# Performance work log

Hardware: AMD Instinct MI355X
Metric: run time of the kernel (lower is better)

Reference implementation:

```python
import jax, jax.numpy as jnp
import numpy as np

NUM_HEADS = 12
HEAD_DIM = 64
NPT = 1  # num_prefix_tokens

def _rot(x):
    # pairs (x0,x1) -> (-x1, x0), matching timm's rot()
    x2 = x.reshape(*x.shape[:-1], -1, 2)
    r = jnp.stack([-x2[..., 1], x2[..., 0]], axis=-1)
    return r.reshape(x.shape)

def _apply_rope_cat(x, rope):
    # rope: [N_rot, 2*hd] = sin||cos concatenated
    sin, cos = jnp.split(rope, 2, axis=-1)
    return x * cos + _rot(x) * sin

def setup_inputs() -> dict:
    key = jax.random.key(0)
    ks = jax.random.split(key, 7)
    B, N, C = 8, 4097, 768
    hd = HEAD_DIM
    x = jax.random.normal(ks[0], (B, N, C), jnp.float32)
    rope = jax.random.normal(ks[1], (N - NPT, 2 * hd), jnp.float32)
    qkv_w = jax.random.normal(ks[2], (3 * C, C), jnp.float32) * (C ** -0.5)
    q_bias = jax.random.normal(ks[3], (C,), jnp.float32) * 0.02
    v_bias = jax.random.normal(ks[4], (C,), jnp.float32) * 0.02
    proj_w = jax.random.normal(ks[5], (C, C), jnp.float32) * (C ** -0.5)
    proj_b = jax.random.normal(ks[6], (C,), jnp.float32) * 0.02
    return dict(x=x, rope=rope, qkv_w=qkv_w, q_bias=q_bias, v_bias=v_bias,
                proj_w=proj_w, proj_b=proj_b)

def reference(x, rope, qkv_w, q_bias, v_bias, proj_w, proj_b):
    B, N, C = x.shape
    H, hd = NUM_HEADS, HEAD_DIM
    # fused QKV with k_bias fixed at zero (non-trainable buffer)
    bias = jnp.concatenate([q_bias, jnp.zeros_like(q_bias), v_bias])
    qkv = x @ qkv_w.T + bias                            # [B,N,3C]
    qkv = qkv.reshape(B, N, 3, H, hd).transpose(2, 0, 3, 1, 4)
    q, k, v = qkv[0], qkv[1], qkv[2]                    # [B,H,N,hd]
    # RoPE on all tokens except the prefix (CLS) token
    q = jnp.concatenate([q[:, :, :NPT], _apply_rope_cat(q[:, :, NPT:], rope)], axis=2)
    k = jnp.concatenate([k[:, :, :NPT], _apply_rope_cat(k[:, :, NPT:], rope)], axis=2)
    # linear attention: kv = K^T V, then Q @ kv, normalized by hd*N
    kv = jnp.einsum('bhnd,bhne->bhde', k, v)            # [B,H,hd,hd]
    out = jnp.einsum('bhnd,bhde->bhne', q, kv) / hd / N # [B,H,N,hd]
    out = out.transpose(0, 2, 1, 3).reshape(B, N, C)
    return out @ proj_w.T + proj_b
```

## Files before the change

### kernel.cpp

```cpp
#include <hip/hip_runtime.h>
#include <hip/hip_bf16.h>

typedef __attribute__((ext_vector_type(8))) short short8;
typedef __attribute__((ext_vector_type(4))) float f32x4;

#define B_    8
#define N_    4097
#define C_    768
#define M_TOT (B_*N_)
#define K3    (3*C_)
#define CHUNKS 16
#define NSTEP 24

__device__ __forceinline__ float bf2f(unsigned short u) {
  union { unsigned int i; float f; } x; x.i = ((unsigned int)u) << 16; return x.f;
}
__device__ __forceinline__ unsigned short f2bf(float f) {
  union { float f; unsigned int i; } x; x.f = f;
  unsigned int i = x.i + 0x7fffu + ((x.i >> 16) & 1u);
  return (unsigned short)(i >> 16);
}
__device__ __forceinline__ void gload16(const void* g, void* l) {
  __builtin_amdgcn_global_load_lds(
      (const __attribute__((address_space(1))) void*)g,
      (__attribute__((address_space(3))) void*)l, 16, 0, 0);
}

__global__ __launch_bounds__(256) void cvt_kernel(const float* __restrict__ inx,
                                                  unsigned short* __restrict__ outx,
                                                  const float* __restrict__ inw,
                                                  unsigned short* __restrict__ outw,
                                                  long n4x, long n4tot) {
  long i = (long)blockIdx.x * blockDim.x + threadIdx.x;
  long stride = (long)gridDim.x * blockDim.x;
  for (; i < n4tot; i += stride) {
    const float4* src; ushort4* dst; long j;
    if (i < n4x) { src = (const float4*)inx; dst = (ushort4*)outx; j = i; }
    else         { src = (const float4*)inw; dst = (ushort4*)outw; j = i - n4x; }
    float4 v = src[j];
    ushort4 o;
    o.x = f2bf(v.x); o.y = f2bf(v.y); o.z = f2bf(v.z); o.w = f2bf(v.w);
    dst[j] = o;
  }
}

__global__ __launch_bounds__(512, 4) void gemm_qkv_rope(
    const unsigned short* __restrict__ A,
    const unsigned short* __restrict__ Bw,
    const float* __restrict__ rope,
    const float* __restrict__ qb,
    const float* __restrict__ vb,
    unsigned short* __restrict__ qkv)
{
  __shared__ __align__(16) char L[3*24576];
  const int tid  = threadIdx.x;
  const int wave = tid >> 6, lane = tid & 63;
  const int lr = lane & 15, lk = lane >> 4;
  const int wm = wave >> 2, wn = wave & 3;

  const int o = blockIdx.x;
  const int xcd = o & 7, loc = o >> 3;
  const int tile = (xcd < 1 ? xcd*290 : 290 + (xcd-1)*289) + loc;
  const int m0 = (tile % 257) * 128;
  const int n0 = (tile / 257) * 256;

  const int arow = tid >> 2, achk = tid & 3;
  const int am = min(m0 + arow, M_TOT-1);
  const unsigned short* gA  = A  + (long)am*768 + achk*8;
  const unsigned short* gB1 = Bw + (long)(n0 + arow)*768 + achk*8;
  const unsigned short* gB2 = Bw + (long)(n0 + arow + 128)*768 + achk*8;
  const int dA  = wave*1024;
  const int dB1 = 8192  + wave*1024;
  const int dB2 = 16384 + wave*1024;

  const int abase = (wm*64 + lr)*64 + lk*16;
  const int bbase = 8192 + (wn*64 + lr)*64 + lk*16;

  f32x4 acc[4][4];
#pragma unroll
  for (int i = 0; i < 4; ++i)
#pragma unroll
    for (int j = 0; j < 4; ++j) acc[i][j] = (f32x4){0.f,0.f,0.f,0.f};

  auto STAGE = [&](int buf, int kk) {
    char* sb = L + buf*24576;
    gload16(gA  + kk, sb + dA);
    gload16(gB1 + kk, sb + dB1);
    gload16(gB2 + kk, sb + dB2);
  };
  auto COMPUTE = [&](int buf) {
    const char* sb = L + buf*24576;
    short8 af[4], bfr[4];
#pragma unroll
    for (int mi = 0; mi < 4; ++mi)
      af[mi] = *(const short8*)(sb + abase + mi*1024);
#pragma unroll
    for (int ni = 0; ni < 4; ++ni)
      bfr[ni] = *(const short8*)(sb + bbase + ni*1024);
#pragma unroll
    for (int mi = 0; mi < 4; ++mi)
#pragma unroll
      for (int ni = 0; ni < 4; ++ni)
        acc[mi][ni] = __builtin_amdgcn_mfma_f32_16x16x32_bf16(af[mi], bfr[ni], acc[mi][ni], 0, 0, 0);
  };

  STAGE(0, 0);
  STAGE(1, 32);
  asm volatile("s_waitcnt vmcnt(3)" ::: "memory");
  __builtin_amdgcn_s_barrier();
  __builtin_amdgcn_sched_barrier(0);

  int cur = 0;
  for (int tt = 0; tt < NSTEP-2; ++tt) {
    int stg = cur + 2; if (stg >= 3) stg -= 3;
    STAGE(stg, (tt+2)*32);
    COMPUTE(cur);
    asm volatile("s_waitcnt vmcnt(3)" ::: "memory");
    __builtin_amdgcn_sched_barrier(0);
    __builtin_amdgcn_s_barrier();
    __builtin_amdgcn_sched_barrier(0);
    cur = (cur + 1 == 3) ? 0 : cur + 1;
  }
  COMPUTE(cur);
  asm volatile("s_waitcnt vmcnt(0)" ::: "memory");
  __builtin_amdgcn_sched_barrier(0);
  __builtin_amdgcn_s_barrier();
  __builtin_amdgcn_sched_barrier(0);
  cur = (cur + 1 == 3) ? 0 : cur + 1;
  COMPUTE(cur);

  const int which = n0 / 768;
  unsigned short* plane = qkv + (long)which*M_TOT*768;

  float biasv[4]; int withv[4]; int dv[4];
#pragma unroll
  for (int ni = 0; ni < 4; ++ni) {
    const int gc = n0 + wn*64 + ni*16 + lr;
    const int within = gc - which*768;
    withv[ni] = within;
    dv[ni] = within & 63;
    biasv[ni] = (which == 0) ? qb[within] : (which == 2 ? vb[within] : 0.f);
  }

  if (which == 2) {
#pragma unroll
    for (int mi = 0; mi < 4; ++mi)
#pragma unroll
      for (int r = 0; r < 4; ++r) {
        const int gm = m0 + wm*64 + mi*16 + lk*4 + r;
        if (gm < M_TOT) {
#pragma unroll
          for (int ni = 0; ni < 4; ++ni)
            plane[(long)gm*768 + withv[ni]] = f2bf(acc[mi][ni][r] + biasv[ni]);
        }
      }
  } else {
#pragma unroll
    for (int mi = 0; mi < 4; ++mi) {
#pragma unroll
      for (int r = 0; r < 4; ++r) {
        const int gm = m0 + wm*64 + mi*16 + lk*4 + r;
        const int ntok = gm % 4097;
        const bool valid = gm < M_TOT;
        const bool dorope = (ntok > 0) && valid;
        const float* rp = rope + (long)(ntok - 1)*128;
#pragma unroll
        for (int ni = 0; ni < 4; ++ni) {
          float v = acc[mi][ni][r] + biasv[ni];
          float pair = __shfl_xor(v, 1);
          float vo = v;
          if (dorope) {
            const float s = rp[dv[ni]], c = rp[64 + dv[ni]];
            const float rot = (dv[ni] & 1) ? pair : -pair;
            vo = v*c + rot*s;
          }
          if (valid) plane[(long)gm*768 + withv[ni]] = f2bf(vo);
        }
      }
    }
  }
}

__global__ __launch_bounds__(256) void kv_partial_kernel(
    const unsigned short* __restrict__ qkv, float* __restrict__ part)
{
  const int bh = blockIdx.y;
  const int b = bh / 12, h = bh % 12;
  const int chunk = blockIdx.x;
  const int per = (N_ + CHUNKS - 1) / CHUNKS;
  const int nst = chunk * per;
  const int nen = min(nst + per, N_);
  const unsigned short* Kpl = qkv + (long)M_TOT*768 + ((long)b*N_)*768 + h*64;
  const unsigned short* Vpl = qkv + (long)2*M_TOT*768 + ((long)b*N_)*768 + h*64;
  __shared__ unsigned short Kl[32*64];
  __shared__ unsigned short Vl[32*64];
  const int t = threadIdx.x;
  const int ty = t >> 4, tx = t & 15;
  const int lrow = t >> 3, lpc = t & 7;
  float acc[4][4] = {};
  for (int nb = nst; nb < nen; nb += 32) {
    const int cnt = min(32, nen - nb);
    __syncthreads();
    if (lrow < cnt) {
      *(uint4*)(Kl + lrow*64 + lpc*8) = *(const uint4*)(Kpl + (long)(nb + lrow)*768 + lpc*8);
      *(uint4*)(Vl + lrow*64 + lpc*8) = *(const uint4*)(Vpl + (long)(nb + lrow)*768 + lpc*8);
    }
    __syncthreads();
#pragma unroll 2
    for (int i = 0; i < cnt; ++i) {
      const ushort4 ku = *(const ushort4*)(Kl + i*64 + ty*4);
      const ushort4 vu = *(const ushort4*)(Vl + i*64 + tx*4);
      float kf[4] = {bf2f(ku.x), bf2f(ku.y), bf2f(ku.z), bf2f(ku.w)};
      float vf[4] = {bf2f(vu.x), bf2f(vu.y), bf2f(vu.z), bf2f(vu.w)};
#pragma unroll
      for (int a = 0; a < 4; ++a)
#pragma unroll
        for (int e = 0; e < 4; ++e) acc[a][e] += kf[a]*vf[e];
    }
  }
  float* dst = part + ((long)chunk*96 + bh)*4096 + (ty*4)*64 + tx*4;
#pragma unroll
  for (int a = 0; a < 4; ++a)
#pragma unroll
    for (int e = 0; e < 4; ++e) dst[a*64 + e] = acc[a][e];
}

__global__ __launch_bounds__(256) void mcomb_kernel(const float* __restrict__ part,
                                                    const float* __restrict__ pw,
                                                    unsigned short* __restrict__ McT) {
  const int blk = blockIdx.x;
  const int cs = blk & 1;
  const int h  = (blk >> 1) % 12;
  const int b  = blk / 24;
  const int bh = b*12 + h;
  __shared__ float kvs[64][65];
  const int t = threadIdx.x;
  const int d_own = t >> 2;
  const int eg = (t & 3) * 16;

  float4 a0 = {0,0,0,0}, a1 = {0,0,0,0}, a2 = {0,0,0,0}, a3 = {0,0,0,0};
  const float4* p4 = (const float4*)part;
#pragma unroll
  for (int ch = 0; ch < CHUNKS; ++ch) {
    const long base = ((long)ch*96 + bh)*1024 + d_own*16 + (t & 3)*4;
    float4 v0 = p4[base+0], v1 = p4[base+1], v2 = p4[base+2], v3 = p4[base+3];
    a0.x += v0.x; a0.y += v0.y; a0.z += v0.z; a0.w += v0.w;
    a1.x += v1.x; a1.y += v1.y; a1.z += v1.z; a1.w += v1.w;
    a2.x += v2.x; a2.y += v2.y; a2.z += v2.z; a2.w += v2.w;
    a3.x += v3.x; a3.y += v3.y; a3.z += v3.z; a3.w += v3.w;
  }
  kvs[eg+ 0][d_own] = a0.x; kvs[eg+ 1][d_own] = a0.y; kvs[eg+ 2][d_own] = a0.z; kvs[eg+ 3][d_own] = a0.w;
  kvs[eg+ 4][d_own] = a1.x; kvs[eg+ 5][d_own] = a1.y; kvs[eg+ 6][d_own] = a1.z; kvs[eg+ 7][d_own] = a1.w;
  kvs[eg+ 8][d_own] = a2.x; kvs[eg+ 9][d_own] = a2.y; kvs[eg+10][d_own] = a2.z; kvs[eg+11][d_own] = a2.w;
  kvs[eg+12][d_own] = a3.x; kvs[eg+13][d_own] = a3.y; kvs[eg+14][d_own] = a3.z; kvs[eg+15][d_own] = a3.w;
  __syncthreads();

  const int lane = t & 63;
  const int w    = t >> 6;
  float kvcol[64];
#pragma unroll
  for (int e = 0; e < 64; ++e) kvcol[e] = kvs[e][lane];

  const float scale = (float)(1.0/(64.0*4097.0));
  const int cbase = cs*384 + w*96;
  for (int i = 0; i < 96; ++i) {
    const int c = cbase + i;
    const float* pwrow = pw + (long)c*768 + h*64;
    float s = 0.f;
#pragma unroll
    for (int e = 0; e < 64; ++e) s += pwrow[e] * kvcol[e];
    McT[((long)b*768 + c)*768 + h*64 + lane] = f2bf(s * scale);
  }
}

__global__ __launch_bounds__(512, 4) void gemm_final(
    const unsigned short* __restrict__ qkv,
    const unsigned short* __restrict__ McT,
    const float* __restrict__ pb,
    float* __restrict__ out)
{
  __shared__ __align__(16) char L[3*24576];
  const int tid  = threadIdx.x;
  const int wave = tid >> 6, lane = tid & 63;
  const int lr = lane & 15, lk = lane >> 4;
  const int wm = wave >> 2, wn = wave & 3;

  const int o = blockIdx.x;
  const int xcd = o & 7, loc = o >> 3;
  const int b  = xcd;
  const int ct = loc / 33, mt = loc % 33;
  const int m0 = mt * 128;
  const int c0 = ct * 256;

  const int arow = tid >> 2, achk = tid & 3;
  const int am = min(m0 + arow, N_-1);
  const unsigned short* gA  = qkv + ((long)b*N_ + am)*768 + achk*8;
  const unsigned short* Bb  = McT + (long)b*768*768;
  const unsigned short* gB1 = Bb + (long)(c0 + arow)*768 + achk*8;
  const unsigned short* gB2 = Bb + (long)(c0 + arow + 128)*768 + achk*8;
  const int dA  = wave*1024;
  const int dB1 = 8192  + wave*1024;
  const int dB2 = 16384 + wave*1024;

  const int abase = (wm*64 + lr)*64 + lk*16;
  const int bbase = 8192 + (wn*64 + lr)*64 + lk*16;

  f32x4 acc[4][4];
#pragma unroll
  for (int i = 0; i < 4; ++i)
#pragma unroll
    for (int j = 0; j < 4; ++j) acc[i][j] = (f32x4){0.f,0.f,0.f,0.f};

  auto STAGE = [&](int buf, int kk) {
    char* sb = L + buf*24576;
    gload16(gA  + kk, sb + dA);
    gload16(gB1 + kk, sb + dB1);
    gload16(gB2 + kk, sb + dB2);
  };
  auto COMPUTE = [&](int buf) {
    const char* sb = L + buf*24576;
    short8 af[4], bfr[4];
#pragma unroll
    for (int mi = 0; mi < 4; ++mi)
      af[mi] = *(const short8*)(sb + abase + mi*1024);
#pragma unroll
    for (int ni = 0; ni < 4; ++ni)
      bfr[ni] = *(const short8*)(sb + bbase + ni*1024);
#pragma unroll
    for (int mi = 0; mi < 4; ++mi)
#pragma unroll
      for (int ni = 0; ni < 4; ++ni)
        acc[mi][ni] = __builtin_amdgcn_mfma_f32_16x16x32_bf16(af[mi], bfr[ni], acc[mi][ni], 0, 0, 0);
  };

  STAGE(0, 0);
  STAGE(1, 32);
  asm volatile("s_waitcnt vmcnt(3)" ::: "memory");
  __builtin_amdgcn_s_barrier();
  __builtin_amdgcn_sched_barrier(0);

  int cur = 0;
  for (int tt = 0; tt < NSTEP-2; ++tt) {
    int stg = cur + 2; if (stg >= 3) stg -= 3;
    STAGE(stg, (tt+2)*32);
    COMPUTE(cur);
    asm volatile("s_waitcnt vmcnt(3)" ::: "memory");
    __builtin_amdgcn_sched_barrier(0);
    __builtin_amdgcn_s_barrier();
    __builtin_amdgcn_sched_barrier(0);
    cur = (cur + 1 == 3) ? 0 : cur + 1;
  }
  COMPUTE(cur);
  asm volatile("s_waitcnt vmcnt(0)" ::: "memory");
  __builtin_amdgcn_sched_barrier(0);
  __builtin_amdgcn_s_barrier();
  __builtin_amdgcn_sched_barrier(0);
  cur = (cur + 1 == 3) ? 0 : cur + 1;
  COMPUTE(cur);

#pragma unroll
  for (int mi = 0; mi < 4; ++mi) {
#pragma unroll
    for (int ni = 0; ni < 4; ++ni) {
      const int gc = c0 + wn*64 + ni*16 + lr;
      const float bias = pb[gc];
#pragma unroll
      for (int r = 0; r < 4; ++r) {
        const int tok = m0 + wm*64 + mi*16 + lk*4 + r;
        if (tok < N_)
          out[((long)b*N_ + tok)*768 + gc] = acc[mi][ni][r] + bias;
      }
    }
  }
}

extern "C" void kernel_launch(void* const* d_in, const int* in_sizes, int n_in,
                              void* d_out, int out_size, void* d_ws, size_t ws_size,
                              hipStream_t stream) {
  const float* x      = (const float*)d_in[0];
  const float* rope   = (const float*)d_in[1];
  const float* qkv_w  = (const float*)d_in[2];
  const float* q_bias = (const float*)d_in[3];
  const float* v_bias = (const float*)d_in[4];
  const float* proj_w = (const float*)d_in[5];
  const float* proj_b = (const float*)d_in[6];
  float* out = (float*)d_out;

  char* w0 = (char*)d_ws;
  unsigned short* x_bf  = (unsigned short*)w0;
  unsigned short* wq_bf = (unsigned short*)(w0 + 50343936);
  unsigned short* qkv   = (unsigned short*)(w0 + 50343936 + 3538944);
  float*          part  = (float*)w0;
  unsigned short* McT   = (unsigned short*)(w0 + 25165824 + 1572864);

  const long n4x = (long)M_TOT*768/4;
  const long n4w = (long)K3*768/4;
  cvt_kernel<<<2048, 256, 0, stream>>>(x, x_bf, qkv_w, wq_bf, n4x, n4x + n4w);

  gemm_qkv_rope<<<2313, 512, 0, stream>>>(x_bf, wq_bf, rope, q_bias, v_bias, qkv);

  kv_partial_kernel<<<dim3(CHUNKS, 96), 256, 0, stream>>>(qkv, part);
  mcomb_kernel<<<192, 256, 0, stream>>>(part, proj_w, McT);

  gemm_final<<<792, 512, 0, stream>>>(qkv, McT, proj_b, out);
}
```

Measured before the change: 438.1 us.

## Reorder LDS tile layout to MFMA fragment order, swap tile raster, use nontemporal stores

Both GEMM kernels now stage A/B tiles into LDS so that each wave's 16-row by 32-k block is stored contiguously in lane order. Fragment reads become linear per lane, which is meant to avoid LDS bank conflicts. The tile index mapping changes from M-major to N-major within each XCD, so neighbouring blocks reuse the same A rows in L2. Output stores use nontemporal hints to reduce cache pollution, which risks slower re-reads of qkv by later kernels.

```diff
diff --git a/kernel.cpp b/kernel.cpp
--- a/kernel.cpp
+++ b/kernel.cpp
@@ -61,20 +61,21 @@
   const int o = blockIdx.x;
   const int xcd = o & 7, loc = o >> 3;
   const int tile = (xcd < 1 ? xcd*290 : 290 + (xcd-1)*289) + loc;
-  const int m0 = (tile % 257) * 128;
-  const int n0 = (tile / 257) * 256;
-
-  const int arow = tid >> 2, achk = tid & 3;
+  const int m0 = (tile / 9) * 128;
+  const int n0 = (tile % 9) * 256;
+
+  const int arow = wave*16 + lr;
+  const int achk = lk;
   const int am = min(m0 + arow, M_TOT-1);
   const unsigned short* gA  = A  + (long)am*768 + achk*8;
   const unsigned short* gB1 = Bw + (long)(n0 + arow)*768 + achk*8;
-  const unsigned short* gB2 = Bw + (long)(n0 + arow + 128)*768 + achk*8;
-  const int dA  = wave*1024;
-  const int dB1 = 8192  + wave*1024;
-  const int dB2 = 16384 + wave*1024;
-
-  const int abase = (wm*64 + lr)*64 + lk*16;
-  const int bbase = 8192 + (wn*64 + lr)*64 + lk*16;
+  const unsigned short* gB2 = Bw + (long)(n0 + 128 + arow)*768 + achk*8;
+  const int dA  = tid*16;
+  const int dB1 = 8192  + tid*16;
+  const int dB2 = 16384 + tid*16;
+
+  const int abase = (wm*4)*1024 + lane*16;
+  const int bbase = 8192 + (wn*4)*1024 + lane*16;
 
   f32x4 acc[4][4];
 #pragma unroll
@@ -151,7 +152,8 @@
         if (gm < M_TOT) {
 #pragma unroll
           for (int ni = 0; ni < 4; ++ni)
-            plane[(long)gm*768 + withv[ni]] = f2bf(acc[mi][ni][r] + biasv[ni]);
+            __builtin_nontemporal_store(f2bf(acc[mi][ni][r] + biasv[ni]),
+                                        plane + (long)gm*768 + withv[ni]);
         }
       }
   } else {
@@ -174,7 +176,8 @@
             const float rot = (dv[ni] & 1) ? pair : -pair;
             vo = v*c + rot*s;
           }
-          if (valid) plane[(long)gm*768 + withv[ni]] = f2bf(vo);
+          if (valid)
+            __builtin_nontemporal_store(f2bf(vo), plane + (long)gm*768 + withv[ni]);
         }
       }
     }
@@ -288,22 +291,23 @@
   const int o = blockIdx.x;
   const int xcd = o & 7, loc = o >> 3;
   const int b  = xcd;
-  const int ct = loc / 33, mt = loc % 33;
+  const int mt = loc / 3, ct = loc % 3;
   const int m0 = mt * 128;
   const int c0 = ct * 256;
 
-  const int arow = tid >> 2, achk = tid & 3;
+  const int arow = wave*16 + lr;
+  const int achk = lk;
   const int am = min(m0 + arow, N_-1);
   const unsigned short* gA  = qkv + ((long)b*N_ + am)*768 + achk*8;
   const unsigned short* Bb  = McT + (long)b*768*768;
   const unsigned short* gB1 = Bb + (long)(c0 + arow)*768 + achk*8;
-  const unsigned short* gB2 = Bb + (long)(c0 + arow + 128)*768 + achk*8;
-  const int dA  = wave*1024;
-  const int dB1 = 8192  + wave*1024;
-  const int dB2 = 16384 + wave*1024;
-
-  const int abase = (wm*64 + lr)*64 + lk*16;
-  const int bbase = 8192 + (wn*64 + lr)*64 + lk*16;
+  const unsigned short* gB2 = Bb + (long)(c0 + 128 + arow)*768 + achk*8;
+  const int dA  = tid*16;
+  const int dB1 = 8192  + tid*16;
+  const int dB2 = 16384 + tid*16;
+
+  const int abase = (wm*4)*1024 + lane*16;
+  const int bbase = 8192 + (wn*4)*1024 + lane*16;
 
   f32x4 acc[4][4];
 #pragma unroll
@@ -368,7 +372,8 @@
       for (int r = 0; r < 4; ++r) {
         const int tok = m0 + wm*64 + mi*16 + lk*4 + r;
         if (tok < N_)
-          out[((long)b*N_ + tok)*768 + gc] = acc[mi][ni][r] + bias;
+          __builtin_nontemporal_store(acc[mi][ni][r] + bias,
+                                      out + ((long)b*N_ + tok)*768 + gc);
       }
     }
   }
```

Result: slower. 476.6 us (+8.8%).
